# Kernel optimization log

Hardware: AMD Instinct MI355X
Metric: run time of the kernel (lower is better)

Reference implementation:

```python
import jax, jax.numpy as jnp
import numpy as np

H = 300      # hidden_dim == GloVe embedding dim (LSTM output is discarded)
MID = 100    # Scorer hidden width
N = 1024     # sentence length


def setup_inputs() -> dict:
    key = jax.random.key(0)
    k1, k2, k3, k4, k5, k6 = jax.random.split(key, 6)
    sentence = jax.random.normal(k1, (N, H), dtype=jnp.float32)
    target_scores = jax.random.randint(k2, (N,), 0, N + 1)
    # nn.Linear(2H, MID) and nn.Linear(MID, 1) params (uniform fan-in init style)
    lim1 = 1.0 / np.sqrt(2 * H)
    W1 = jax.random.uniform(k3, (MID, 2 * H), dtype=jnp.float32, minval=-lim1, maxval=lim1)
    b1 = jax.random.uniform(k4, (MID,), dtype=jnp.float32, minval=-lim1, maxval=lim1)
    lim2 = 1.0 / np.sqrt(MID)
    W2 = jax.random.uniform(k5, (1, MID), dtype=jnp.float32, minval=-lim2, maxval=lim2)
    b2 = jax.random.uniform(k6, (1,), dtype=jnp.float32, minval=-lim2, maxval=lim2)
    return {"sentence": sentence, "target_scores": target_scores,
            "W1": W1, "b1": b1, "W2": W2, "b2": b2}


def reference(sentence, W1, b1, W2, b2, target_scores):
    n = sentence.shape[0]
    # potential_matches = [zeros(H); sentence] -> [n+1, H]
    pm = jnp.concatenate([jnp.zeros((1, H), sentence.dtype), sentence], axis=0)
    # Split the first Linear over the two concatenated halves and broadcast-add:
    # cat(sentence[i], pm[j]) @ W1^T == sentence[i] @ W1[:, :H]^T + pm[j] @ W1[:, H:]^T
    s1 = jnp.einsum('nh,mh->nm', sentence, W1[:, :H])   # [n, MID]
    s2 = jnp.einsum('ph,mh->pm', pm, W1[:, H:])          # [n+1, MID]
    hidden = jax.nn.sigmoid(s1[:, None, :] + s2[None, :, :] + b1)  # [n, n+1, MID]
    scores = jnp.einsum('npm,om->npo', hidden, W2)[..., 0] + b2[0]  # [n, n+1]
    # L1 loss against one-hot indicator of the true head, averaged over all pairs
    indicator = (jnp.arange(n + 1)[None, :] == target_scores[:, None]).astype(scores.dtype)
    loss = jnp.mean(jnp.abs(scores - indicator))
    score_matrix = jax.nn.softmax(scores, axis=1)
    return loss, score_matrix
```

## Files before the change

kernel.cpp:

```cpp
#include <hip/hip_runtime.h>

#define H     300
#define MID   100
#define NN    1024
#define NP1   1025
#define SST   1088

__global__ __launch_bounds__(256) void precompute_kernel(
    const float* __restrict__ sentence,
    const float* __restrict__ W1,
    const float* __restrict__ b1,
    float* __restrict__ s1b,
    float* __restrict__ s2T,
    float* __restrict__ out)
{
    __shared__ float rA[H];
    __shared__ float rB[H];
    const int tid = threadIdx.x;
    const int iA = blockIdx.x * 2, iB = iA + 1;

    if (blockIdx.x == 0) {
        if (tid == 0) out[0] = 0.0f;
        if (tid < MID) s2T[(long)tid * SST] = 0.0f;
    }

    const float* sA = sentence + (long)iA * H;
    const float* sB = sentence + (long)iB * H;
    for (int idx = tid; idx < 2 * H; idx += 256) {
        if (idx < H) rA[idx] = sA[idx];
        else         rB[idx - H] = sB[idx - H];
    }
    __syncthreads();

    const int wv   = tid >> 6;
    const int lane = tid & 63;
    const int sub  = lane >> 5;
    const int hb   = lane & 31;
    const int half = wv >> 1;
    const int mb   = (wv & 1) * 50;

    for (int q = 0; q < 25; ++q) {
        const int m = mb + 2 * q + sub;
        const float* wrow = W1 + (long)m * (2 * H) + half * H;
        float aA = 0.f, aB = 0.f;
        #pragma unroll
        for (int k = 0; k < 9; ++k) {
            const int h = hb + 32 * k;
            const float w = wrow[h];
            aA = __builtin_fmaf(w, rA[h], aA);
            aB = __builtin_fmaf(w, rB[h], aB);
        }
        if (hb < 12) {
            const int h = hb + 288;
            const float w = wrow[h];
            aA = __builtin_fmaf(w, rA[h], aA);
            aB = __builtin_fmaf(w, rB[h], aB);
        }
        #pragma unroll
        for (int off = 16; off > 0; off >>= 1) {
            aA += __shfl_xor(aA, off, 64);
            aB += __shfl_xor(aB, off, 64);
        }
        if (hb == 0) {
            if (half == 0) {
                const float bb = b1[m];
                s1b[iA * MID + m] = aA + bb;
                s1b[iB * MID + m] = aB + bb;
            } else {
                s2T[(long)m * SST + (iA + 1)] = aA;
                s2T[(long)m * SST + (iB + 1)] = aB;
            }
        }
    }
}

__global__ __launch_bounds__(1024, 4) void main_kernel(
    const float* __restrict__ s1b,
    const float* __restrict__ s2T,
    const float* __restrict__ W2,
    const float* __restrict__ b2,
    const int*   __restrict__ target,
    float* __restrict__ out)
{
    __shared__ float4 Fq[MID];
    __shared__ float2 w2sh[MID / 2];
    __shared__ float  tmp[4][104];
    __shared__ float  redl[16];
    __shared__ float4 redm[16];
    __shared__ float4 rede[16];
    __shared__ float  sc4sh[4];
    __shared__ float4 bmax, binv;

    const int i0  = blockIdx.x * 4;
    const int tid = threadIdx.x;
    const int lane = tid & 63, wv = tid >> 6;
    const float NL  = -1.4426950408889634f;
    const float L2E =  1.4426950408889634f;

    if (tid < MID) {
        Fq[tid] = make_float4(
            __builtin_amdgcn_exp2f(s1b[(i0 + 0) * MID + tid] * NL),
            __builtin_amdgcn_exp2f(s1b[(i0 + 1) * MID + tid] * NL),
            __builtin_amdgcn_exp2f(s1b[(i0 + 2) * MID + tid] * NL),
            __builtin_amdgcn_exp2f(s1b[(i0 + 3) * MID + tid] * NL));
    } else if (tid >= 128 && tid < 128 + MID / 2) {
        const int p = tid - 128;
        w2sh[p] = make_float2(W2[2 * p], W2[2 * p + 1]);
    }
    const float b2v = b2[0];
    __syncthreads();

    const float* col = s2T + tid;
    #define LDX(m) col[(long)(m) * SST]

    float a0 = 0.f, a1 = 0.f, a2 = 0.f, a3 = 0.f;

    #define PBODY(p_, X0, X1)                                              \
        do {                                                               \
            const float E0 = __builtin_amdgcn_exp2f((X0) * NL);            \
            const float E1 = __builtin_amdgcn_exp2f((X1) * NL);            \
            const float4 F0 = Fq[2 * (p_)];                                \
            const float4 F1 = Fq[2 * (p_) + 1];                            \
            const float2 w  = w2sh[p_];                                    \
            {                                                              \
                const float A = __builtin_fmaf(E0, F0.x, 1.f);             \
                const float B = __builtin_fmaf(E1, F1.x, 1.f);             \
                a0 = __builtin_fmaf(__builtin_fmaf(w.x, B, w.y * A),       \
                                    __builtin_amdgcn_rcpf(A * B), a0);     \
            }                                                              \
            {                                                              \
                const float A = __builtin_fmaf(E0, F0.y, 1.f);             \
                const float B = __builtin_fmaf(E1, F1.y, 1.f);             \
                a1 = __builtin_fmaf(__builtin_fmaf(w.x, B, w.y * A),       \
                                    __builtin_amdgcn_rcpf(A * B), a1);     \
            }                                                              \
            {                                                              \
                const float A = __builtin_fmaf(E0, F0.z, 1.f);             \
                const float B = __builtin_fmaf(E1, F1.z, 1.f);             \
                a2 = __builtin_fmaf(__builtin_fmaf(w.x, B, w.y * A),       \
                                    __builtin_amdgcn_rcpf(A * B), a2);     \
            }                                                              \
            {                                                              \
                const float A = __builtin_fmaf(E0, F0.w, 1.f);             \
                const float B = __builtin_fmaf(E1, F1.w, 1.f);             \
                a3 = __builtin_fmaf(__builtin_fmaf(w.x, B, w.y * A),       \
                                    __builtin_amdgcn_rcpf(A * B), a3);     \
            }                                                              \
        } while (0)

    float x0 = LDX(0), x1 = LDX(1), x2 = LDX(2), x3 = LDX(3);
    #pragma unroll 2
    for (int p = 0; p < 48; ++p) {
        const float xn0 = LDX(2 * p + 4);
        const float xn1 = LDX(2 * p + 5);
        PBODY(p, x0, x1);
        x0 = x2; x1 = x3; x2 = xn0; x3 = xn1;
    }
    PBODY(48, x0, x1);
    PBODY(49, x2, x3);

    const float sc0 = a0 + b2v, sc1 = a1 + b2v, sc2 = a2 + b2v, sc3 = a3 + b2v;

    if (tid < MID) {
        const float x = s2T[(long)tid * SST + 1024];
        const float E = __builtin_amdgcn_exp2f(x * NL);
        const float4 F = Fq[tid];
        const float wm = W2[tid];
        tmp[0][tid] = wm * __builtin_amdgcn_rcpf(__builtin_fmaf(E, F.x, 1.f));
        tmp[1][tid] = wm * __builtin_amdgcn_rcpf(__builtin_fmaf(E, F.y, 1.f));
        tmp[2][tid] = wm * __builtin_amdgcn_rcpf(__builtin_fmaf(E, F.z, 1.f));
        tmp[3][tid] = wm * __builtin_amdgcn_rcpf(__builtin_fmaf(E, F.w, 1.f));
    }
    __syncthreads();
    if (wv < 4) {
        float v = tmp[wv][lane] + ((lane < MID - 64) ? tmp[wv][lane + 64] : 0.f);
        #pragma unroll
        for (int off = 32; off > 0; off >>= 1) v += __shfl_down(v, off);
        if (lane == 0) sc4sh[wv] = v + b2v;
    }
    __syncthreads();

    const int tg0 = target[i0], tg1 = target[i0 + 1];
    const int tg2 = target[i0 + 2], tg3 = target[i0 + 3];
    float ls = fabsf(sc0 - ((tid == tg0) ? 1.f : 0.f))
             + fabsf(sc1 - ((tid == tg1) ? 1.f : 0.f))
             + fabsf(sc2 - ((tid == tg2) ? 1.f : 0.f))
             + fabsf(sc3 - ((tid == tg3) ? 1.f : 0.f));
    float4 mx = make_float4(sc0, sc1, sc2, sc3);
    if (tid == 0) {
        ls += fabsf(sc4sh[0] - ((1024 == tg0) ? 1.f : 0.f))
            + fabsf(sc4sh[1] - ((1024 == tg1) ? 1.f : 0.f))
            + fabsf(sc4sh[2] - ((1024 == tg2) ? 1.f : 0.f))
            + fabsf(sc4sh[3] - ((1024 == tg3) ? 1.f : 0.f));
        mx.x = fmaxf(mx.x, sc4sh[0]);
        mx.y = fmaxf(mx.y, sc4sh[1]);
        mx.z = fmaxf(mx.z, sc4sh[2]);
        mx.w = fmaxf(mx.w, sc4sh[3]);
    }
    #pragma unroll
    for (int off = 32; off > 0; off >>= 1) {
        ls += __shfl_down(ls, off);
        mx.x = fmaxf(mx.x, __shfl_down(mx.x, off));
        mx.y = fmaxf(mx.y, __shfl_down(mx.y, off));
        mx.z = fmaxf(mx.z, __shfl_down(mx.z, off));
        mx.w = fmaxf(mx.w, __shfl_down(mx.w, off));
    }
    if (lane == 0) { redl[wv] = ls; redm[wv] = mx; }
    __syncthreads();
    if (tid == 0) {
        float L = 0.f;
        float4 M = make_float4(-1e30f, -1e30f, -1e30f, -1e30f);
        #pragma unroll
        for (int k = 0; k < 16; ++k) {
            L += redl[k];
            M.x = fmaxf(M.x, redm[k].x);
            M.y = fmaxf(M.y, redm[k].y);
            M.z = fmaxf(M.z, redm[k].z);
            M.w = fmaxf(M.w, redm[k].w);
        }
        atomicAdd(out, L * (1.0f / ((float)NN * (float)NP1)));
        bmax = M;
    }
    __syncthreads();
    const float4 rm = bmax;

    const float e0 = __builtin_amdgcn_exp2f((sc0 - rm.x) * L2E);
    const float e1 = __builtin_amdgcn_exp2f((sc1 - rm.y) * L2E);
    const float e2 = __builtin_amdgcn_exp2f((sc2 - rm.z) * L2E);
    const float e3 = __builtin_amdgcn_exp2f((sc3 - rm.w) * L2E);
    float4 e4v = make_float4(0.f, 0.f, 0.f, 0.f);
    if (tid == 0) {
        e4v.x = __builtin_amdgcn_exp2f((sc4sh[0] - rm.x) * L2E);
        e4v.y = __builtin_amdgcn_exp2f((sc4sh[1] - rm.y) * L2E);
        e4v.z = __builtin_amdgcn_exp2f((sc4sh[2] - rm.z) * L2E);
        e4v.w = __builtin_amdgcn_exp2f((sc4sh[3] - rm.w) * L2E);
    }
    float4 es = make_float4(e0 + e4v.x, e1 + e4v.y, e2 + e4v.z, e3 + e4v.w);
    #pragma unroll
    for (int off = 32; off > 0; off >>= 1) {
        es.x += __shfl_down(es.x, off);
        es.y += __shfl_down(es.y, off);
        es.z += __shfl_down(es.z, off);
        es.w += __shfl_down(es.w, off);
    }
    if (lane == 0) rede[wv] = es;
    __syncthreads();
    if (tid == 0) {
        float4 S = make_float4(0.f, 0.f, 0.f, 0.f);
        #pragma unroll
        for (int k = 0; k < 16; ++k) {
            S.x += rede[k].x; S.y += rede[k].y;
            S.z += rede[k].z; S.w += rede[k].w;
        }
        binv = make_float4(1.f / S.x, 1.f / S.y, 1.f / S.z, 1.f / S.w);
    }
    __syncthreads();
    const float4 iv = binv;

    float* o0 = out + 1 + (long)(i0 + 0) * NP1;
    float* o1 = out + 1 + (long)(i0 + 1) * NP1;
    float* o2 = out + 1 + (long)(i0 + 2) * NP1;
    float* o3 = out + 1 + (long)(i0 + 3) * NP1;
    o0[tid] = e0 * iv.x;
    o1[tid] = e1 * iv.y;
    o2[tid] = e2 * iv.z;
    o3[tid] = e3 * iv.w;
    if (tid == 0) {
        o0[1024] = e4v.x * iv.x;
        o1[1024] = e4v.y * iv.y;
        o2[1024] = e4v.z * iv.z;
        o3[1024] = e4v.w * iv.w;
    }
    #undef PBODY
    #undef LDX
}

extern "C" void kernel_launch(void* const* d_in, const int* in_sizes, int n_in,
                              void* d_out, int out_size, void* d_ws, size_t ws_size,
                              hipStream_t stream) {
    const float* sentence = (const float*)d_in[0];
    const int*   target   = (const int*)  d_in[1];
    const float* W1       = (const float*)d_in[2];
    const float* b1       = (const float*)d_in[3];
    const float* W2       = (const float*)d_in[4];
    const float* b2       = (const float*)d_in[5];
    float* out = (float*)d_out;

    float* s1b = (float*)d_ws;
    float* s2T = s1b + NN * MID;

    precompute_kernel<<<NN / 2, 256, 0, stream>>>(sentence, W1, b1, s1b, s2T, out);
    main_kernel<<<NN / 4, 1024, 0, stream>>>(s1b, s2T, W2, b2, target, out);
}
```

Baseline: 106.6 us.

## Precompute exp of s2 and batch four sigmoids per reciprocal with float4 layout

The precompute kernel now stores exp(-s2) directly instead of raw s2, so the main kernel no longer evaluates an exp per (j,m) element for every row block. The s2 workspace is relaid out as groups of four MID values per column so each thread fetches them with a single float4 load. The inner loop combines four sigmoid terms over a common denominator, issuing one reciprocal per four terms instead of one per two. This trades transcendental and load instructions for extra multiplies, and the larger products in the shared denominator carry some risk of overflow or precision loss.

```diff
diff --git a/kernel.cpp b/kernel.cpp
--- a/kernel.cpp
+++ b/kernel.cpp
@@ -4,24 +4,26 @@
 #define MID   100
 #define NN    1024
 #define NP1   1025
-#define SST   1088
+#define JST   1088
 
 __global__ __launch_bounds__(256) void precompute_kernel(
     const float* __restrict__ sentence,
     const float* __restrict__ W1,
     const float* __restrict__ b1,
     float* __restrict__ s1b,
-    float* __restrict__ s2T,
+    float* __restrict__ E4,
     float* __restrict__ out)
 {
     __shared__ float rA[H];
     __shared__ float rB[H];
     const int tid = threadIdx.x;
     const int iA = blockIdx.x * 2, iB = iA + 1;
+    const float NL = -1.4426950408889634f;
 
     if (blockIdx.x == 0) {
         if (tid == 0) out[0] = 0.0f;
-        if (tid < MID) s2T[(long)tid * SST] = 0.0f;
+        if (tid < MID)
+            E4[(long)((tid >> 2) * JST) * 4 + (tid & 3)] = 1.0f;
     }
 
     const float* sA = sentence + (long)iA * H;
@@ -67,8 +69,9 @@
                 s1b[iA * MID + m] = aA + bb;
                 s1b[iB * MID + m] = aB + bb;
             } else {
-                s2T[(long)m * SST + (iA + 1)] = aA;
-                s2T[(long)m * SST + (iB + 1)] = aB;
+                float* base = E4 + (long)((m >> 2) * JST) * 4 + (m & 3);
+                base[(long)(iA + 1) * 4] = __builtin_amdgcn_exp2f(aA * NL);
+                base[(long)(iB + 1) * 4] = __builtin_amdgcn_exp2f(aB * NL);
             }
         }
     }
@@ -76,14 +79,14 @@
 
 __global__ __launch_bounds__(1024, 4) void main_kernel(
     const float* __restrict__ s1b,
-    const float* __restrict__ s2T,
+    const float* __restrict__ E4,
     const float* __restrict__ W2,
     const float* __restrict__ b2,
     const int*   __restrict__ target,
     float* __restrict__ out)
 {
     __shared__ float4 Fq[MID];
-    __shared__ float2 w2sh[MID / 2];
+    __shared__ float4 w4sh[MID / 4];
     __shared__ float  tmp[4][104];
     __shared__ float  redl[16];
     __shared__ float4 redm[16];
@@ -103,67 +106,84 @@
             __builtin_amdgcn_exp2f(s1b[(i0 + 1) * MID + tid] * NL),
             __builtin_amdgcn_exp2f(s1b[(i0 + 2) * MID + tid] * NL),
             __builtin_amdgcn_exp2f(s1b[(i0 + 3) * MID + tid] * NL));
-    } else if (tid >= 128 && tid < 128 + MID / 2) {
+    } else if (tid >= 128 && tid < 128 + MID / 4) {
         const int p = tid - 128;
-        w2sh[p] = make_float2(W2[2 * p], W2[2 * p + 1]);
+        w4sh[p] = make_float4(W2[4 * p], W2[4 * p + 1], W2[4 * p + 2], W2[4 * p + 3]);
     }
     const float b2v = b2[0];
     __syncthreads();
 
-    const float* col = s2T + tid;
-    #define LDX(m) col[(long)(m) * SST]
+    #define LDX(p_) (*(const float4*)(E4 + ((long)(p_) * JST + tid) * 4))
 
     float a0 = 0.f, a1 = 0.f, a2 = 0.f, a3 = 0.f;
 
-    #define PBODY(p_, X0, X1)                                              \
-        do {                                                               \
-            const float E0 = __builtin_amdgcn_exp2f((X0) * NL);            \
-            const float E1 = __builtin_amdgcn_exp2f((X1) * NL);            \
-            const float4 F0 = Fq[2 * (p_)];                                \
-            const float4 F1 = Fq[2 * (p_) + 1];                            \
-            const float2 w  = w2sh[p_];                                    \
-            {                                                              \
-                const float A = __builtin_fmaf(E0, F0.x, 1.f);             \
-                const float B = __builtin_fmaf(E1, F1.x, 1.f);             \
-                a0 = __builtin_fmaf(__builtin_fmaf(w.x, B, w.y * A),       \
-                                    __builtin_amdgcn_rcpf(A * B), a0);     \
-            }                                                              \
-            {                                                              \
-                const float A = __builtin_fmaf(E0, F0.y, 1.f);             \
-                const float B = __builtin_fmaf(E1, F1.y, 1.f);             \
-                a1 = __builtin_fmaf(__builtin_fmaf(w.x, B, w.y * A),       \
-                                    __builtin_amdgcn_rcpf(A * B), a1);     \
-            }                                                              \
-            {                                                              \
-                const float A = __builtin_fmaf(E0, F0.z, 1.f);             \
-                const float B = __builtin_fmaf(E1, F1.z, 1.f);             \
-                a2 = __builtin_fmaf(__builtin_fmaf(w.x, B, w.y * A),       \
-                                    __builtin_amdgcn_rcpf(A * B), a2);     \
-            }                                                              \
-            {                                                              \
-                const float A = __builtin_fmaf(E0, F0.w, 1.f);             \
-                const float B = __builtin_fmaf(E1, F1.w, 1.f);             \
-                a3 = __builtin_fmaf(__builtin_fmaf(w.x, B, w.y * A),       \
-                                    __builtin_amdgcn_rcpf(A * B), a3);     \
-            }                                                              \
+    #define QBODY(p_, X)                                                     \
+        do {                                                                 \
+            const float4 F0 = Fq[4 * (p_)];                                  \
+            const float4 F1 = Fq[4 * (p_) + 1];                              \
+            const float4 F2 = Fq[4 * (p_) + 2];                              \
+            const float4 F3 = Fq[4 * (p_) + 3];                              \
+            const float4 w  = w4sh[p_];                                      \
+            {                                                                \
+                const float A = __builtin_fmaf((X).x, F0.x, 1.f);            \
+                const float B = __builtin_fmaf((X).y, F1.x, 1.f);            \
+                const float C = __builtin_fmaf((X).z, F2.x, 1.f);            \
+                const float D = __builtin_fmaf((X).w, F3.x, 1.f);            \
+                const float AB = A * B, CD = C * D;                          \
+                const float R = __builtin_amdgcn_rcpf(AB * CD);              \
+                const float n1 = __builtin_fmaf(w.x, B, w.y * A);            \
+                const float n2 = __builtin_fmaf(w.z, D, w.w * C);            \
+                a0 = __builtin_fmaf(__builtin_fmaf(n1, CD, n2 * AB), R, a0); \
+            }                                                                \
+            {                                                                \
+                const float A = __builtin_fmaf((X).x, F0.y, 1.f);            \
+                const float B = __builtin_fmaf((X).y, F1.y, 1.f);            \
+                const float C = __builtin_fmaf((X).z, F2.y, 1.f);            \
+                const float D = __builtin_fmaf((X).w, F3.y, 1.f);            \
+                const float AB = A * B, CD = C * D;                          \
+                const float R = __builtin_amdgcn_rcpf(AB * CD);              \
+                const float n1 = __builtin_fmaf(w.x, B, w.y * A);            \
+                const float n2 = __builtin_fmaf(w.z, D, w.w * C);            \
+                a1 = __builtin_fmaf(__builtin_fmaf(n1, CD, n2 * AB), R, a1); \
+            }                                                                \
+            {                                                                \
+                const float A = __builtin_fmaf((X).x, F0.z, 1.f);            \
+                const float B = __builtin_fmaf((X).y, F1.z, 1.f);            \
+                const float C = __builtin_fmaf((X).z, F2.z, 1.f);            \
+                const float D = __builtin_fmaf((X).w, F3.z, 1.f);            \
+                const float AB = A * B, CD = C * D;                          \
+                const float R = __builtin_amdgcn_rcpf(AB * CD);              \
+                const float n1 = __builtin_fmaf(w.x, B, w.y * A);            \
+                const float n2 = __builtin_fmaf(w.z, D, w.w * C);            \
+                a2 = __builtin_fmaf(__builtin_fmaf(n1, CD, n2 * AB), R, a2); \
+            }                                                                \
+            {                                                                \
+                const float A = __builtin_fmaf((X).x, F0.w, 1.f);            \
+                const float B = __builtin_fmaf((X).y, F1.w, 1.f);            \
+                const float C = __builtin_fmaf((X).z, F2.w, 1.f);            \
+                const float D = __builtin_fmaf((X).w, F3.w, 1.f);            \
+                const float AB = A * B, CD = C * D;                          \
+                const float R = __builtin_amdgcn_rcpf(AB * CD);              \
+                const float n1 = __builtin_fmaf(w.x, B, w.y * A);            \
+                const float n2 = __builtin_fmaf(w.z, D, w.w * C);            \
+                a3 = __builtin_fmaf(__builtin_fmaf(n1, CD, n2 * AB), R, a3); \
+            }                                                                \
         } while (0)
 
-    float x0 = LDX(0), x1 = LDX(1), x2 = LDX(2), x3 = LDX(3);
-    #pragma unroll 2
-    for (int p = 0; p < 48; ++p) {
-        const float xn0 = LDX(2 * p + 4);
-        const float xn1 = LDX(2 * p + 5);
-        PBODY(p, x0, x1);
-        x0 = x2; x1 = x3; x2 = xn0; x3 = xn1;
-    }
-    PBODY(48, x0, x1);
-    PBODY(49, x2, x3);
+    float4 x0 = LDX(0), x1 = LDX(1);
+    #pragma unroll 4
+    for (int p = 0; p < 23; ++p) {
+        const float4 xn = LDX(p + 2);
+        QBODY(p, x0);
+        x0 = x1; x1 = xn;
+    }
+    QBODY(23, x0);
+    QBODY(24, x1);
 
     const float sc0 = a0 + b2v, sc1 = a1 + b2v, sc2 = a2 + b2v, sc3 = a3 + b2v;
 
     if (tid < MID) {
-        const float x = s2T[(long)tid * SST + 1024];
-        const float E = __builtin_amdgcn_exp2f(x * NL);
+        const float E = E4[((long)(tid >> 2) * JST + 1024) * 4 + (tid & 3)];
         const float4 F = Fq[tid];
         const float wm = W2[tid];
         tmp[0][tid] = wm * __builtin_amdgcn_rcpf(__builtin_fmaf(E, F.x, 1.f));
@@ -271,7 +291,7 @@
         o2[1024] = e4v.z * iv.z;
         o3[1024] = e4v.w * iv.w;
     }
-    #undef PBODY
+    #undef QBODY
     #undef LDX
 }
 
@@ -287,8 +307,8 @@
     float* out = (float*)d_out;
 
     float* s1b = (float*)d_ws;
-    float* s2T = s1b + NN * MID;
-
-    precompute_kernel<<<NN / 2, 256, 0, stream>>>(sentence, W1, b1, s1b, s2T, out);
-    main_kernel<<<NN / 4, 1024, 0, stream>>>(s1b, s2T, W2, b2, target, out);
+    float* E4  = s1b + NN * MID;
+
+    precompute_kernel<<<NN / 2, 256, 0, stream>>>(sentence, W1, b1, s1b, E4, out);
+    main_kernel<<<NN / 4, 1024, 0, stream>>>(s1b, E4, W2, b2, target, out);
 }
```

Measured after the change: 102.7 us. 1.04x faster.
